# Optimization experiments

Measured on AMD Instinct MI355X. Metric: run time of the kernel, lower is better.

## Reference

```python
import jax, jax.numpy as jnp
import numpy as np

HEADS = 8
EPS = 1e-5


def dwconv(x, w):
    # x: [B, C, L], w: [C, 1, K] depthwise kernel (groups == C), 'same' padding (K odd)
    K = w.shape[-1]
    p = (K - 1) // 2
    return jax.lax.conv_general_dilated(
        x, w, window_strides=(1,), padding=[(p, p)],
        dimension_numbers=('NCH', 'OIH', 'NCH'),
        feature_group_count=x.shape[1])


def dds_conv(x, pw, dw3, dw15, gate):
    # DynamicDepthSeparableConv1d: 1x1 pointwise (no bias) -> two depthwise convs
    # combined with softmax-gated weighted sum.
    o = jnp.einsum('oc,bcl->bol', pw, x)
    g = jax.nn.softmax(gate)
    return g[0] * dwconv(o, dw3) + g[1] * dwconv(o, dw15)


def instance_norm(x, gamma, beta):
    # InstanceNorm1d(affine=True), biased variance over length dim
    m = jnp.mean(x, axis=-1, keepdims=True)
    v = jnp.mean((x - m) ** 2, axis=-1, keepdims=True)
    return (x - m) * jax.lax.rsqrt(v + EPS) * gamma[None, :, None] + beta[None, :, None]


def block(x, p):
    B, C, L = x.shape
    h = HEADS
    Q = dds_conv(x, p['pw_q'], p['dw3_q'], p['dw15_q'], p['gate_q']).reshape(B, h, C, L)
    K = dds_conv(x, p['pw_k'], p['dw3_k'], p['dw15_k'], p['gate_k']).reshape(B, h, C, L)
    V = dds_conv(x, p['pw_v'], p['dw3_v'], p['dw15_v'], p['gate_v']).reshape(B, h, C, L)
    scale = C ** -0.25
    # dot[b,h,k,q] = sum_c K[b,h,c,k] * Q[b,h,c,q]; softmax over key dim (axis=2)
    dot = jnp.einsum('bhck,bhcq->bhkq', K * scale, Q * scale)
    attn = jax.nn.softmax(dot, axis=2)
    o = jnp.einsum('bhck,bhkq->bhcq', V, attn).reshape(B, h * C, L)
    attended = jnp.einsum('oc,bcl->bol', p['uni_W'], o) + p['uni_b'][None, :, None]
    # dropout is identity at inference
    x = instance_norm(attended + x, p['n1_g'], p['n1_b'])
    h1 = jax.nn.relu(jnp.einsum('oc,bcl->bol', p['ffn_W1'], x) + p['ffn_b1'][None, :, None])
    ff = jnp.einsum('oc,bcl->bol', p['ffn_W2'], h1) + p['ffn_b2'][None, :, None]
    x = instance_norm(ff + x, p['n2_g'], p['n2_b'])
    return x


def setup_inputs() -> dict:
    key = jax.random.key(0)
    ks = jax.random.split(key, 32)
    D, C, h, L, B, IN = 6, 32, HEADS, 2048, 8, 6
    CH = C * h
    s = 0.05
    inp = {
        'x': jax.random.normal(ks[0], (B, IN, L), jnp.float32),
        'enc_W': jax.random.normal(ks[1], (C, IN), jnp.float32) * s,
        'enc_b': jnp.zeros((C,), jnp.float32),
        'pw_q': jax.random.normal(ks[2], (D, CH, C), jnp.float32) * s,
        'dw3_q': jax.random.normal(ks[3], (D, CH, 1, 3), jnp.float32) * s,
        'dw15_q': jax.random.normal(ks[4], (D, CH, 1, 15), jnp.float32) * s,
        'gate_q': jnp.ones((D, 2), jnp.float32),
        'pw_k': jax.random.normal(ks[5], (D, CH, C), jnp.float32) * s,
        'dw3_k': jax.random.normal(ks[6], (D, CH, 1, 3), jnp.float32) * s,
        'dw15_k': jax.random.normal(ks[7], (D, CH, 1, 15), jnp.float32) * s,
        'gate_k': jnp.ones((D, 2), jnp.float32),
        'pw_v': jax.random.normal(ks[8], (D, CH, C), jnp.float32) * s,
        'dw3_v': jax.random.normal(ks[9], (D, CH, 1, 3), jnp.float32) * s,
        'dw15_v': jax.random.normal(ks[10], (D, CH, 1, 15), jnp.float32) * s,
        'gate_v': jnp.ones((D, 2), jnp.float32),
        'uni_W': jax.random.normal(ks[11], (D, C, CH), jnp.float32) * s,
        'uni_b': jnp.zeros((D, C), jnp.float32),
        'n1_g': jnp.ones((D, C), jnp.float32),
        'n1_b': jnp.zeros((D, C), jnp.float32),
        'n2_g': jnp.ones((D, C), jnp.float32),
        'n2_b': jnp.zeros((D, C), jnp.float32),
        'ffn_W1': jax.random.normal(ks[12], (D, 4 * C, C), jnp.float32) * s,
        'ffn_b1': jnp.zeros((D, 4 * C), jnp.float32),
        'ffn_W2': jax.random.normal(ks[13], (D, C, 4 * C), jnp.float32) * s,
        'ffn_b2': jnp.zeros((D, C), jnp.float32),
        'cls_W': jax.random.normal(ks[14], (1, C), jnp.float32) * s,
        'cls_b': jnp.zeros((1,), jnp.float32),
    }
    return inp


def reference(x, enc_W, enc_b, pw_q, dw3_q, dw15_q, gate_q, pw_k, dw3_k, dw15_k,
              gate_k, pw_v, dw3_v, dw15_v, gate_v, uni_W, uni_b, n1_g, n1_b,
              n2_g, n2_b, ffn_W1, ffn_b1, ffn_W2, ffn_b2, cls_W, cls_b):
    h = jnp.einsum('oc,bcl->bol', enc_W, x) + enc_b[None, :, None]
    params = dict(pw_q=pw_q, dw3_q=dw3_q, dw15_q=dw15_q, gate_q=gate_q,
                  pw_k=pw_k, dw3_k=dw3_k, dw15_k=dw15_k, gate_k=gate_k,
                  pw_v=pw_v, dw3_v=dw3_v, dw15_v=dw15_v, gate_v=gate_v,
                  uni_W=uni_W, uni_b=uni_b, n1_g=n1_g, n1_b=n1_b,
                  n2_g=n2_g, n2_b=n2_b, ffn_W1=ffn_W1, ffn_b1=ffn_b1,
                  ffn_W2=ffn_W2, ffn_b2=ffn_b2)
    def step(carry, p):
        return block(carry, p), None
    h, _ = jax.lax.scan(step, h, params)
    logits = jnp.einsum('oc,bcl->bol', cls_W, h) + cls_b[None, :, None]  # [B,1,L]
    return jax.nn.sigmoid(logits)[:, 0, :]  # strong (per-timestep) probabilities [B, L]
```

## Files before the change

kernel.cpp:

```cpp
#include <hip/hip_runtime.h>
#include <math.h>

#define LL   2048
#define BB   8
#define CC   32
#define CHH  256
#define HH   8
#define DD   6

typedef _Float16 h8 __attribute__((ext_vector_type(8)));
typedef _Float16 h4 __attribute__((ext_vector_type(4)));
typedef float f4 __attribute__((ext_vector_type(4)));
typedef float f2v __attribute__((ext_vector_type(2)));

__global__ __launch_bounds__(256) void k_enc(const float* __restrict__ x,
    const float* __restrict__ W, const float* __restrict__ bias,
    float* __restrict__ X) {
  int idx = blockIdx.x * 256 + threadIdx.x;
  int l = idx & (LL - 1);
  int c = (idx >> 11) & 31;
  int b = idx >> 16;
  float s = bias[c];
#pragma unroll
  for (int i = 0; i < 6; ++i)
    s = fmaf(W[c * 6 + i], x[((size_t)b * 6 + i) * LL + l], s);
  X[idx] = s;
}

__global__ __launch_bounds__(256) void k_qkv(const float* __restrict__ X,
    const float* __restrict__ pwq, const float* __restrict__ pwk,
    const float* __restrict__ pwv,
    const float* __restrict__ d3q, const float* __restrict__ d15q, const float* __restrict__ gq,
    const float* __restrict__ d3k, const float* __restrict__ d15k, const float* __restrict__ gk,
    const float* __restrict__ d3v, const float* __restrict__ d15v, const float* __restrict__ gv,
    _Float16* __restrict__ Qt, _Float16* __restrict__ Kt, _Float16* __restrict__ Vt) {
  __shared__ __align__(16) char lds[21504];
  int z  = blockIdx.y;
  int bx = blockIdx.x;
  int bh = bx >> 4, lt = bx & 15, l0 = lt * 128;
  int b = bh >> 3, h = bh & 7;
  int t = threadIdx.x;
  const float* pwp  = (z == 0) ? pwq  : (z == 1) ? pwk  : pwv;
  const float* w3p  = (z == 0) ? d3q  : (z == 1) ? d3k  : d3v;
  const float* w15p = (z == 0) ? d15q : (z == 1) ? d15k : d15v;
  const float* gp   = (z == 0) ? gq   : (z == 1) ? gk   : gv;

  char* Xh = lds;
  char* Wh = lds + 9728;
  char* ot = lds + 11776;

  {
    int r = t >> 3, u = t & 7;
    const float* xr = X + ((size_t)b * CC + r) * LL;
    char* xd = Xh + r * 304;
#pragma unroll
    for (int s = u; s < 36; s += 8) {
      int ls = l0 - 8 + s * 4;
      f4 v;
      if (ls >= 0 && ls + 3 < LL) {
        v = *(const f4*)(xr + ls);
      } else {
#pragma unroll
        for (int e = 0; e < 4; ++e) {
          int l = ls + e;
          v[e] = (l >= 0 && l < LL) ? xr[l] : 0.f;
        }
      }
      uint2 pk;
      pk.x = __builtin_bit_cast(unsigned, __builtin_amdgcn_cvt_pkrtz(v[0], v[1]));
      pk.y = __builtin_bit_cast(unsigned, __builtin_amdgcn_cvt_pkrtz(v[2], v[3]));
      *(uint2*)(xd + s * 8) = pk;
    }
  }
  {
    f4 wg = ((const f4*)(pwp + h * 1024))[t];
    uint2 pk;
    pk.x = __builtin_bit_cast(unsigned, __builtin_amdgcn_cvt_pkrtz(wg[0], wg[1]));
    pk.y = __builtin_bit_cast(unsigned, __builtin_amdgcn_cvt_pkrtz(wg[2], wg[3]));
    *(uint2*)(Wh + (t >> 3) * 64 + (t & 7) * 8) = pk;
  }
  __syncthreads();

  {
    int w4 = t >> 6, lane = t & 63;
    int g = lane >> 4, ln = lane & 15;
    h8 af[2];
#pragma unroll
    for (int mt = 0; mt < 2; ++mt)
      af[mt] = *(const h8*)(Wh + (mt * 16 + ln) * 64 + g * 16);
    for (int nt = w4; nt < 9; nt += 4) {
      h8 bf;
#pragma unroll
      for (int j = 0; j < 8; ++j)
        bf[j] = *(const _Float16*)(Xh + (g * 8 + j) * 304 + (nt * 16 + ln) * 2);
#pragma unroll
      for (int mt = 0; mt < 2; ++mt) {
        f4 zr = {0.f, 0.f, 0.f, 0.f};
        f4 d = __builtin_amdgcn_mfma_f32_16x16x32_f16(af[mt], bf, zr, 0, 0, 0);
#pragma unroll
        for (int i = 0; i < 4; ++i)
          *(_Float16*)(ot + (mt * 16 + g * 4 + i) * 304 + (nt * 16 + ln) * 2) =
              (_Float16)d[i];
      }
    }
  }
  __syncthreads();

  int c = t & 31, cg = t >> 5;
  float wv[32];
  {
    const h8* wp = (const h8*)(ot + c * 304 + cg * 32);
#pragma unroll
    for (int q4 = 0; q4 < 4; ++q4) {
      h8 v = wp[q4];
#pragma unroll
      for (int e = 0; e < 8; ++e) wv[q4 * 8 + e] = (float)v[e];
    }
  }
  float r0 = gp[0], r1 = gp[1];
  float mx = fmaxf(r0, r1);
  float e0 = __expf(r0 - mx), e1 = __expf(r1 - mx);
  float gi = 1.f / (e0 + e1);
  float g0 = e0 * gi, g1 = e1 * gi;
  float sc = (z == 0) ? 0.2550765737f : 1.0f;
  int ch = h * 32 + c;
  float w3r[3], w15r[15];
#pragma unroll
  for (int k = 0; k < 3; ++k)  w3r[k]  = w3p[ch * 3 + k];
#pragma unroll
  for (int k = 0; k < 15; ++k) w15r[k] = w15p[ch * 15 + k];

  h8 olo, ohi;
#pragma unroll
  for (int i = 0; i < 16; ++i) {
    float a = 0.f;
#pragma unroll
    for (int k = 0; k < 3; ++k) a = fmaf(w3r[k], wv[i + 7 + k], a);
    float s15 = 0.f;
#pragma unroll
    for (int k = 0; k < 15; ++k) s15 = fmaf(w15r[k], wv[i + 1 + k], s15);
    float val = (g0 * a + g1 * s15) * sc;
    if (i < 8) olo[i] = (_Float16)val; else ohi[i - 8] = (_Float16)val;
  }

  if (z == 2) {
    _Float16* dst = Vt + ((size_t)bh * 32 + c) * LL + l0 + cg * 16;
    *(h8*)dst = olo;
    *(h8*)(dst + 8) = ohi;
  } else {
    char* tb = lds;
    __syncthreads();
#pragma unroll
    for (int i = 0; i < 16; ++i) {
      _Float16 v = (i < 8) ? olo[i] : ohi[i - 8];
      *(_Float16*)(tb + (cg * 16 + i) * 80 + c * 2) = v;
    }
    __syncthreads();
    _Float16* dst = ((z == 0) ? Qt : Kt) + ((size_t)bh * LL + l0) * 32;
    int l = t >> 1, hf = t & 1;
    uint4 a = *(uint4*)(tb + l * 80 + hf * 32);
    uint4 b2 = *(uint4*)(tb + l * 80 + hf * 32 + 16);
    *(uint4*)(dst + (size_t)l * 32 + hf * 16) = a;
    *(uint4*)(dst + (size_t)l * 32 + hf * 16 + 8) = b2;
  }
}

__global__ __launch_bounds__(512, 2) void k_attn(
    const _Float16* __restrict__ Qt, const _Float16* __restrict__ Kt,
    const _Float16* __restrict__ Vt, _Float16* __restrict__ AO) {
  __shared__ __align__(16) char lds[38912];
  const int tid  = threadIdx.x;
  const int lane = tid & 63;
  const int w    = tid >> 6;
  const int seg  = w >> 2;
  const int wq   = w & 3;
  const int g    = lane >> 4;
  const int ln   = lane & 15;
  const int h2c  = (wq >> 1) * 2;
  const int lin  = blockIdx.x + (blockIdx.y << 4);
  const int swz  = ((lin & 7) << 7) | (lin >> 3);
  const int qb   = swz & 15;
  const int bh   = swz >> 4;
  const _Float16* Qg = Qt + ((size_t)bh * LL + qb * 128) * 32;
  const _Float16* Kg = Kt + ((size_t)bh * LL + seg * 1024) * 32;
  const _Float16* Vg = Vt + (size_t)bh * 32 * LL + seg * 1024;

  h8 qf[2];
#pragma unroll
  for (int nt = 0; nt < 2; ++nt)
    qf[nt] = *(const h8*)(Qg + (size_t)(wq * 32 + nt * 16 + ln) * 32 + g * 8);

  h8 ones;
#pragma unroll
  for (int j = 0; j < 8; ++j) ones[j] = (_Float16)1.0f;

  char* kb = lds + seg * 5120;
  char* vb = lds + 20480 + seg * 4608;

  uint4 stg0, stg1;
  if ((wq & 1) == 0) {
    const uint4* gk = (const uint4*)Kg;
    stg0 = gk[h2c * 64 + lane];
    stg1 = gk[(h2c + 1) * 64 + lane];
    *(uint4*)(kb + (h2c * 16 + (lane >> 2)) * 80 + (lane & 3) * 16) = stg0;
    *(uint4*)(kb + ((h2c + 1) * 16 + (lane >> 2)) * 80 + (lane & 3) * 16) = stg1;
  } else {
    int c0 = h2c * 8 + (lane >> 3);
    stg0 = *(const uint4*)(Vg + (size_t)c0 * LL + (lane & 7) * 8);
    stg1 = *(const uint4*)(Vg + (size_t)(c0 + 8) * LL + (lane & 7) * 8);
    *(uint4*)(vb + c0 * 144 + (lane & 7) * 16) = stg0;
    *(uint4*)(vb + (c0 + 8) * 144 + (lane & 7) * 16) = stg1;
  }
  __syncthreads();

  f4 o[2][2];
#pragma unroll
  for (int ct = 0; ct < 2; ++ct)
#pragma unroll
    for (int nt = 0; nt < 2; ++nt) o[ct][nt] = (f4){0.f, 0.f, 0.f, 0.f};
  f4 sacc[2];
#pragma unroll
  for (int nt = 0; nt < 2; ++nt) sacc[nt] = (f4){0.f, 0.f, 0.f, 0.f};

  for (int it = 0; it < 16; ++it) {
    int pp = it & 1;
    char* kbc = kb + pp * 10240;
    char* vbc = vb + pp * 9216;
    if (it < 15) {
      int k0n = (it + 1) * 64;
      if ((wq & 1) == 0) {
        const uint4* gk = (const uint4*)(Kg + (size_t)k0n * 32);
        stg0 = gk[h2c * 64 + lane];
        stg1 = gk[(h2c + 1) * 64 + lane];
      } else {
        int c0 = h2c * 8 + (lane >> 3);
        stg0 = *(const uint4*)(Vg + (size_t)c0 * LL + k0n + (lane & 7) * 8);
        stg1 = *(const uint4*)(Vg + (size_t)(c0 + 8) * LL + k0n + (lane & 7) * 8);
      }
    }
#pragma unroll
    for (int chunk = 0; chunk < 2; ++chunk) {
      unsigned pa[2][2], pb[2][2];
#pragma unroll
      for (int mt2 = 0; mt2 < 2; ++mt2) {
        h8 kf = *(const h8*)(kbc + ((chunk * 2 + mt2) * 16 + ln) * 80 + g * 16);
#pragma unroll
        for (int nt = 0; nt < 2; ++nt) {
          f4 z = {0.f, 0.f, 0.f, 0.f};
          f4 s = __builtin_amdgcn_mfma_f32_16x16x32_f16(kf, qf[nt], z, 0, 0, 0);
          float p0 = __builtin_amdgcn_exp2f(s[0]);
          float p1 = __builtin_amdgcn_exp2f(s[1]);
          float p2 = __builtin_amdgcn_exp2f(s[2]);
          float p3 = __builtin_amdgcn_exp2f(s[3]);
          unsigned lo = __builtin_bit_cast(unsigned,
              __builtin_amdgcn_cvt_pkrtz(p0, p1));
          unsigned hi = __builtin_bit_cast(unsigned,
              __builtin_amdgcn_cvt_pkrtz(p2, p3));
          if (mt2 == 0) { pa[nt][0] = lo; pa[nt][1] = hi; }
          else          { pb[nt][0] = lo; pb[nt][1] = hi; }
        }
      }
      h8 vf[2];
#pragma unroll
      for (int ct = 0; ct < 2; ++ct)
        vf[ct] = *(const h8*)(vbc + (ct * 16 + ln) * 144 + chunk * 64 + g * 16);
#pragma unroll
      for (int nt = 0; nt < 2; ++nt) {
        unsigned w0 = pa[nt][0], w1 = pa[nt][1];
        unsigned w2 = pb[nt][0], w3 = pb[nt][1];
        asm("v_permlane32_swap_b32 %0, %1" : "+v"(w0), "+v"(w2));
        asm("v_permlane16_swap_b32 %0, %1" : "+v"(w0), "+v"(w2));
        asm("v_permlane32_swap_b32 %0, %1" : "+v"(w1), "+v"(w3));
        asm("v_permlane16_swap_b32 %0, %1" : "+v"(w1), "+v"(w3));
        uint4 pw4; pw4.x = w0; pw4.y = w1; pw4.z = w2; pw4.w = w3;
        h8 pf = __builtin_bit_cast(h8, pw4);
        sacc[nt] = __builtin_amdgcn_mfma_f32_16x16x32_f16(ones, pf, sacc[nt], 0, 0, 0);
        o[0][nt] = __builtin_amdgcn_mfma_f32_16x16x32_f16(vf[0], pf, o[0][nt], 0, 0, 0);
        o[1][nt] = __builtin_amdgcn_mfma_f32_16x16x32_f16(vf[1], pf, o[1][nt], 0, 0, 0);
      }
    }
    if (it < 15) {
      char* kbn = kb + (pp ^ 1) * 10240;
      char* vbn = vb + (pp ^ 1) * 9216;
      if ((wq & 1) == 0) {
        *(uint4*)(kbn + (h2c * 16 + (lane >> 2)) * 80 + (lane & 3) * 16) = stg0;
        *(uint4*)(kbn + ((h2c + 1) * 16 + (lane >> 2)) * 80 + (lane & 3) * 16) = stg1;
      } else {
        int c0 = h2c * 8 + (lane >> 3);
        *(uint4*)(vbn + c0 * 144 + (lane & 7) * 16) = stg0;
        *(uint4*)(vbn + (c0 + 8) * 144 + (lane & 7) * 16) = stg1;
      }
    }
    __syncthreads();
  }

  if (seg == 1) {
    char* eo = lds + wq * 9216 + lane * 144;
#pragma unroll
    for (int nt = 0; nt < 2; ++nt)
#pragma unroll
      for (int ct = 0; ct < 2; ++ct)
        *(f4*)(eo + (nt * 2 + ct) * 16) = o[ct][nt];
    f4 sv;
    sv[0] = sacc[0][0]; sv[1] = sacc[1][0];
    sv[2] = 0.f; sv[3] = 0.f;
    *(f4*)(eo + 64) = sv;
  }
  __syncthreads();
  if (seg == 0) {
    const char* po = lds + wq * 9216 + lane * 144;
    f4 s1v = *(const f4*)(po + 64);
    _Float16* out = AO + (size_t)bh * (32 * LL);
#pragma unroll
    for (int nt = 0; nt < 2; ++nt) {
      float inv = 1.f / (sacc[nt][0] + s1v[nt]);
      int qg = qb * 128 + wq * 32 + nt * 16 + ln;
#pragma unroll
      for (int ct = 0; ct < 2; ++ct) {
        f4 o1 = *(const f4*)(po + (nt * 2 + ct) * 16);
#pragma unroll
        for (int r = 0; r < 4; ++r)
          out[(size_t)(ct * 16 + g * 4 + r) * LL + qg] =
              (_Float16)((o[ct][nt][r] + o1[r]) * inv);
      }
    }
  }
}

__global__ __launch_bounds__(256) void k_uni_res(const _Float16* __restrict__ AO,
    const float* __restrict__ W, const float* __restrict__ bias,
    const float* __restrict__ Xin, float* __restrict__ Y) {
  __shared__ __align__(16) char lds[35840];
  char* Wh = lds;
  char* Bh = lds + 17920;
  int t  = threadIdx.x;
  int bx = blockIdx.x;
  int lt = bx & 63, b = bx >> 6;
  int l0 = lt * 32;

#pragma unroll
  for (int i = 0; i < 8; ++i) {
    int idx = t + i * 256;
    f4 wv4 = ((const f4*)W)[idx];
    uint2 pk;
    pk.x = __builtin_bit_cast(unsigned, __builtin_amdgcn_cvt_pkrtz(wv4[0], wv4[1]));
    pk.y = __builtin_bit_cast(unsigned, __builtin_amdgcn_cvt_pkrtz(wv4[2], wv4[3]));
    int c = idx >> 6, ccp = idx & 63;
    *(uint2*)(Wh + c * 560 + ccp * 8) = pk;
  }
#pragma unroll
  for (int it = 0; it < 4; ++it) {
    int cc = it * 64 + (t >> 2), chunk = t & 3;
    h8 av = *(const h8*)(AO + ((size_t)b * CHH + cc) * LL + l0 + chunk * 8);
#pragma unroll
    for (int e = 0; e < 8; ++e)
      *(_Float16*)(Bh + (chunk * 8 + e) * 560 + cc * 2) = av[e];
  }
  __syncthreads();

  int wv = t >> 6, lane = t & 63;
  int g = lane >> 4, ln = lane & 15;
  int mt = wv >> 1, nt2 = wv & 1;
  f4 acc = {0.f, 0.f, 0.f, 0.f};
#pragma unroll
  for (int ks = 0; ks < 8; ++ks) {
    h8 af = *(const h8*)(Wh + (mt * 16 + ln) * 560 + (ks * 32 + g * 8) * 2);
    h8 bf = *(const h8*)(Bh + (nt2 * 16 + ln) * 560 + (ks * 32 + g * 8) * 2);
    acc = __builtin_amdgcn_mfma_f32_16x16x32_f16(af, bf, acc, 0, 0, 0);
  }
#pragma unroll
  for (int i = 0; i < 4; ++i) {
    int c = mt * 16 + g * 4 + i;
    size_t o = ((size_t)b * CC + c) * LL + l0 + nt2 * 16 + ln;
    Y[o] = acc[i] + bias[c] + Xin[o];
  }
}

__global__ __launch_bounds__(512) void k_inorm(const float* __restrict__ Y,
    float* __restrict__ X, const float* __restrict__ g,
    const float* __restrict__ bt) {
  __shared__ float red[16];
  int row = blockIdx.x;
  int c = row & 31;
  const float* y = Y + (size_t)row * LL;
  float v[4];
  float s = 0.f, ss = 0.f;
#pragma unroll
  for (int i = 0; i < 4; ++i) {
    v[i] = y[threadIdx.x + 512 * i];
    s += v[i];
    ss = fmaf(v[i], v[i], ss);
  }
#pragma unroll
  for (int off = 32; off; off >>= 1) {
    s  += __shfl_down(s, off);
    ss += __shfl_down(ss, off);
  }
  int wid = threadIdx.x >> 6;
  if ((threadIdx.x & 63) == 0) { red[wid * 2] = s; red[wid * 2 + 1] = ss; }
  __syncthreads();
  if (threadIdx.x == 0) {
    float rs0 = 0.f, rs1 = 0.f;
#pragma unroll
    for (int i = 0; i < 8; ++i) { rs0 += red[i * 2]; rs1 += red[i * 2 + 1]; }
    red[0] = rs0; red[1] = rs1;
  }
  __syncthreads();
  float mean = red[0] * (1.f / LL);
  float var  = red[1] * (1.f / LL) - mean * mean;
  float rs = rsqrtf(var + 1e-5f) * g[c];
  float bb = bt[c];
#pragma unroll
  for (int i = 0; i < 4; ++i)
    X[(size_t)row * LL + threadIdx.x + 512 * i] = (v[i] - mean) * rs + bb;
}

__global__ __launch_bounds__(256) void k_ffn(const float* __restrict__ X,
    const float* __restrict__ W1, const float* __restrict__ b1,
    const float* __restrict__ W2, const float* __restrict__ b2,
    float* __restrict__ Y) {
  __shared__ __align__(16) char lds[30720];
  char* Xh  = lds;
  char* W1h = lds + 2560;
  char* W2h = lds + 12800;
  char* Hh  = lds + 21504;
  float* b1h = (float*)(lds + 30208);
  int t  = threadIdx.x;
  int bx = blockIdx.x;
  int lt = bx & 63, b = bx >> 6;
  int l0 = lt * 32;

  {
    int c = t >> 3, le0 = (t & 7) * 4;
    f4 v = *(const f4*)(X + ((size_t)b * CC + c) * LL + l0 + le0);
#pragma unroll
    for (int e = 0; e < 4; ++e)
      *(_Float16*)(Xh + (le0 + e) * 80 + c * 2) = (_Float16)v[e];
  }
#pragma unroll
  for (int i = 0; i < 4; ++i) {
    int idx = t + i * 256;
    f4 wv4 = ((const f4*)W1)[idx];
    uint2 pk;
    pk.x = __builtin_bit_cast(unsigned, __builtin_amdgcn_cvt_pkrtz(wv4[0], wv4[1]));
    pk.y = __builtin_bit_cast(unsigned, __builtin_amdgcn_cvt_pkrtz(wv4[2], wv4[3]));
    int o = idx >> 3, cp = idx & 7;
    *(uint2*)(W1h + o * 80 + cp * 8) = pk;
  }
#pragma unroll
  for (int i = 0; i < 4; ++i) {
    int idx = t + i * 256;
    f4 wv4 = ((const f4*)W2)[idx];
    uint2 pk;
    pk.x = __builtin_bit_cast(unsigned, __builtin_amdgcn_cvt_pkrtz(wv4[0], wv4[1]));
    pk.y = __builtin_bit_cast(unsigned, __builtin_amdgcn_cvt_pkrtz(wv4[2], wv4[3]));
    int c = idx >> 5, op = idx & 31;
    *(uint2*)(W2h + c * 272 + op * 8) = pk;
  }
  if (t < 128) b1h[t] = b1[t];
  __syncthreads();

  int w4 = t >> 6, lane = t & 63;
  int g = lane >> 4, ln = lane & 15;

#pragma unroll
  for (int j = 0; j < 4; ++j) {
    int ti = w4 * 4 + j;
    int ot = ti >> 1, lt2 = ti & 1;
    h8 af = *(const h8*)(W1h + (ot * 16 + ln) * 80 + g * 16);
    h8 bf = *(const h8*)(Xh + (lt2 * 16 + ln) * 80 + g * 16);
    f4 zr = {0.f, 0.f, 0.f, 0.f};
    f4 d = __builtin_amdgcn_mfma_f32_16x16x32_f16(af, bf, zr, 0, 0, 0);
#pragma unroll
    for (int i = 0; i < 4; ++i) {
      int o = ot * 16 + g * 4 + i;
      float hv = fmaxf(d[i] + b1h[o], 0.f);
      *(_Float16*)(Hh + (lt2 * 16 + ln) * 272 + o * 2) = (_Float16)hv;
    }
  }
  __syncthreads();

  int ct2 = w4 >> 1, lt2b = w4 & 1;
  f4 acc = {0.f, 0.f, 0.f, 0.f};
#pragma unroll
  for (int ks = 0; ks < 4; ++ks) {
    h8 af = *(const h8*)(W2h + (ct2 * 16 + ln) * 272 + (ks * 32 + g * 8) * 2);
    h8 bf = *(const h8*)(Hh + (lt2b * 16 + ln) * 272 + (ks * 32 + g * 8) * 2);
    acc = __builtin_amdgcn_mfma_f32_16x16x32_f16(af, bf, acc, 0, 0, 0);
  }
#pragma unroll
  for (int i = 0; i < 4; ++i) {
    int c = ct2 * 16 + g * 4 + i;
    size_t o = ((size_t)b * CC + c) * LL + l0 + lt2b * 16 + ln;
    Y[o] = acc[i] + b2[c] + X[o];
  }
}

__global__ __launch_bounds__(256) void k_cls(const float* __restrict__ X,
    const float* __restrict__ W, const float* __restrict__ bias,
    float* __restrict__ out) {
  int idx = blockIdx.x * 256 + threadIdx.x;
  int l = idx & (LL - 1);
  int b = idx >> 11;
  float s = bias[0];
#pragma unroll
  for (int c = 0; c < CC; ++c)
    s = fmaf(W[c], X[((size_t)b * CC + c) * LL + l], s);
  out[idx] = 1.f / (1.f + __expf(-s));
}

extern "C" void kernel_launch(void* const* d_in, const int* in_sizes, int n_in,
                              void* d_out, int out_size, void* d_ws,
                              size_t ws_size, hipStream_t stream) {
  const float* x      = (const float*)d_in[0];
  const float* enc_W  = (const float*)d_in[1];
  const float* enc_b  = (const float*)d_in[2];
  const float* pw_q   = (const float*)d_in[3];
  const float* dw3_q  = (const float*)d_in[4];
  const float* dw15_q = (const float*)d_in[5];
  const float* gate_q = (const float*)d_in[6];
  const float* pw_k   = (const float*)d_in[7];
  const float* dw3_k  = (const float*)d_in[8];
  const float* dw15_k = (const float*)d_in[9];
  const float* gate_k = (const float*)d_in[10];
  const float* pw_v   = (const float*)d_in[11];
  const float* dw3_v  = (const float*)d_in[12];
  const float* dw15_v = (const float*)d_in[13];
  const float* gate_v = (const float*)d_in[14];
  const float* uni_W  = (const float*)d_in[15];
  const float* uni_b  = (const float*)d_in[16];
  const float* n1_g   = (const float*)d_in[17];
  const float* n1_b   = (const float*)d_in[18];
  const float* n2_g   = (const float*)d_in[19];
  const float* n2_b   = (const float*)d_in[20];
  const float* ffn_W1 = (const float*)d_in[21];
  const float* ffn_b1 = (const float*)d_in[22];
  const float* ffn_W2 = (const float*)d_in[23];
  const float* ffn_b2 = (const float*)d_in[24];
  const float* cls_W  = (const float*)d_in[25];
  const float* cls_b  = (const float*)d_in[26];

  float* ws = (float*)d_ws;
  float* X   = ws;
  float* Y   = ws + 524288;
  _Float16* AO = (_Float16*)(ws + 1048576);
  _Float16* Qt = (_Float16*)(ws + 9437184);
  _Float16* Kt = (_Float16*)(ws + 11534336);
  _Float16* Vt = (_Float16*)(ws + 13631488);

  k_enc<<<2048, 256, 0, stream>>>(x, enc_W, enc_b, X);

  for (int d = 0; d < DD; ++d) {
    k_qkv<<<dim3(1024, 3), 256, 0, stream>>>(X,
        pw_q + d * CHH * CC, pw_k + d * CHH * CC, pw_v + d * CHH * CC,
        dw3_q + d * CHH * 3, dw15_q + d * CHH * 15, gate_q + d * 2,
        dw3_k + d * CHH * 3, dw15_k + d * CHH * 15, gate_k + d * 2,
        dw3_v + d * CHH * 3, dw15_v + d * CHH * 15, gate_v + d * 2,
        Qt, Kt, Vt);
    k_attn<<<dim3(16, 64), 512, 0, stream>>>(Qt, Kt, Vt, AO);
    k_uni_res<<<512, 256, 0, stream>>>(AO, uni_W + d * CC * CHH,
                                       uni_b + d * CC, X, Y);
    k_inorm<<<256, 512, 0, stream>>>(Y, X, n1_g + d * CC, n1_b + d * CC);
    k_ffn<<<512, 256, 0, stream>>>(X, ffn_W1 + d * 128 * CC, ffn_b1 + d * 128,
                                   ffn_W2 + d * CC * 128, ffn_b2 + d * CC, Y);
    k_inorm<<<256, 512, 0, stream>>>(Y, X, n2_g + d * CC, n2_b + d * CC);
  }

  k_cls<<<64, 256, 0, stream>>>(X, cls_W, cls_b, (float*)d_out);
}
```

Measured before the change: 610.5 us.

## Fuse instance norm into producer/consumer kernels via atomic per-row statistics

Removes the two standalone instance-norm kernels per layer. The residual-producing kernels now accumulate per-(batch,channel) sum and sum-of-squares with shuffle reductions and atomics. The consuming kernels (qkv, ffn, cls) apply the normalization as a scale/shift when they load their input. This cuts 12 launches and the extra read/write passes over the activations, at the cost of atomic contention, a memset, and the less stable E[x^2]-mean^2 variance computed from atomically summed partials.

```diff
diff --git a/kernel.cpp b/kernel.cpp
--- a/kernel.cpp
+++ b/kernel.cpp
@@ -12,6 +12,15 @@
 typedef _Float16 h4 __attribute__((ext_vector_type(4)));
 typedef float f4 __attribute__((ext_vector_type(4)));
 typedef float f2v __attribute__((ext_vector_type(2)));
+
+__device__ __forceinline__ void norm_params(const float* st, const float* g,
+    const float* bt, int bc, int c, float& scr, float& shr) {
+  float s0 = st[bc * 2], s1 = st[bc * 2 + 1];
+  float mean = s0 * (1.f / LL);
+  float var  = s1 * (1.f / LL) - mean * mean;
+  float q = rsqrtf(var + 1e-5f) * g[c];
+  scr = q; shr = bt[c] - mean * q;
+}
 
 __global__ __launch_bounds__(256) void k_enc(const float* __restrict__ x,
     const float* __restrict__ W, const float* __restrict__ bias,
@@ -27,7 +36,9 @@
   X[idx] = s;
 }
 
-__global__ __launch_bounds__(256) void k_qkv(const float* __restrict__ X,
+__global__ __launch_bounds__(256) void k_qkv(const float* __restrict__ Xin,
+    const float* __restrict__ stin, const float* __restrict__ ng,
+    const float* __restrict__ nb, int hasn,
     const float* __restrict__ pwq, const float* __restrict__ pwk,
     const float* __restrict__ pwv,
     const float* __restrict__ d3q, const float* __restrict__ d15q, const float* __restrict__ gq,
@@ -51,7 +62,9 @@
 
   {
     int r = t >> 3, u = t & 7;
-    const float* xr = X + ((size_t)b * CC + r) * LL;
+    const float* xr = Xin + ((size_t)b * CC + r) * LL;
+    float scr = 1.f, shr = 0.f;
+    if (hasn) norm_params(stin, ng, nb, b * 32 + r, r, scr, shr);
     char* xd = Xh + r * 304;
 #pragma unroll
     for (int s = u; s < 36; s += 8) {
@@ -59,11 +72,13 @@
       f4 v;
       if (ls >= 0 && ls + 3 < LL) {
         v = *(const f4*)(xr + ls);
+#pragma unroll
+        for (int e = 0; e < 4; ++e) v[e] = fmaf(v[e], scr, shr);
       } else {
 #pragma unroll
         for (int e = 0; e < 4; ++e) {
           int l = ls + e;
-          v[e] = (l >= 0 && l < LL) ? xr[l] : 0.f;
+          v[e] = (l >= 0 && l < LL) ? fmaf(xr[l], scr, shr) : 0.f;
         }
       }
       uint2 pk;
@@ -329,10 +344,14 @@
 
 __global__ __launch_bounds__(256) void k_uni_res(const _Float16* __restrict__ AO,
     const float* __restrict__ W, const float* __restrict__ bias,
-    const float* __restrict__ Xin, float* __restrict__ Y) {
-  __shared__ __align__(16) char lds[35840];
+    const float* __restrict__ Ain, const float* __restrict__ stin,
+    const float* __restrict__ png, const float* __restrict__ pnb, int hasn,
+    float* __restrict__ Y, float* __restrict__ stout) {
+  __shared__ __align__(16) char lds[36096];
   char* Wh = lds;
   char* Bh = lds + 17920;
+  float* nsc = (float*)(lds + 35840);
+  float* nsh = nsc + 32;
   int t  = threadIdx.x;
   int bx = blockIdx.x;
   int lt = bx & 63, b = bx >> 6;
@@ -356,6 +375,11 @@
     for (int e = 0; e < 8; ++e)
       *(_Float16*)(Bh + (chunk * 8 + e) * 560 + cc * 2) = av[e];
   }
+  if (t < 32) {
+    float scr = 1.f, shr = 0.f;
+    if (hasn) norm_params(stin, png, pnb, b * 32 + t, t, scr, shr);
+    nsc[t] = scr; nsh[t] = shr;
+  }
   __syncthreads();
 
   int wv = t >> 6, lane = t & 63;
@@ -372,59 +396,36 @@
   for (int i = 0; i < 4; ++i) {
     int c = mt * 16 + g * 4 + i;
     size_t o = ((size_t)b * CC + c) * LL + l0 + nt2 * 16 + ln;
-    Y[o] = acc[i] + bias[c] + Xin[o];
-  }
-}
-
-__global__ __launch_bounds__(512) void k_inorm(const float* __restrict__ Y,
-    float* __restrict__ X, const float* __restrict__ g,
-    const float* __restrict__ bt) {
-  __shared__ float red[16];
-  int row = blockIdx.x;
-  int c = row & 31;
-  const float* y = Y + (size_t)row * LL;
-  float v[4];
-  float s = 0.f, ss = 0.f;
-#pragma unroll
-  for (int i = 0; i < 4; ++i) {
-    v[i] = y[threadIdx.x + 512 * i];
-    s += v[i];
-    ss = fmaf(v[i], v[i], ss);
-  }
-#pragma unroll
-  for (int off = 32; off; off >>= 1) {
-    s  += __shfl_down(s, off);
-    ss += __shfl_down(ss, off);
-  }
-  int wid = threadIdx.x >> 6;
-  if ((threadIdx.x & 63) == 0) { red[wid * 2] = s; red[wid * 2 + 1] = ss; }
-  __syncthreads();
-  if (threadIdx.x == 0) {
-    float rs0 = 0.f, rs1 = 0.f;
-#pragma unroll
-    for (int i = 0; i < 8; ++i) { rs0 += red[i * 2]; rs1 += red[i * 2 + 1]; }
-    red[0] = rs0; red[1] = rs1;
-  }
-  __syncthreads();
-  float mean = red[0] * (1.f / LL);
-  float var  = red[1] * (1.f / LL) - mean * mean;
-  float rs = rsqrtf(var + 1e-5f) * g[c];
-  float bb = bt[c];
-#pragma unroll
-  for (int i = 0; i < 4; ++i)
-    X[(size_t)row * LL + threadIdx.x + 512 * i] = (v[i] - mean) * rs + bb;
-}
-
-__global__ __launch_bounds__(256) void k_ffn(const float* __restrict__ X,
+    float res = fmaf(Ain[o], nsc[c], nsh[c]);
+    float val = acc[i] + bias[c] + res;
+    Y[o] = val;
+    float a = val, v2 = val * val;
+#pragma unroll
+    for (int off = 8; off; off >>= 1) {
+      a  += __shfl_down(a, off, 16);
+      v2 += __shfl_down(v2, off, 16);
+    }
+    if (ln == 0) {
+      atomicAdd(&stout[(b * 32 + c) * 2], a);
+      atomicAdd(&stout[(b * 32 + c) * 2 + 1], v2);
+    }
+  }
+}
+
+__global__ __launch_bounds__(256) void k_ffn(const float* __restrict__ Y1,
+    const float* __restrict__ st1, const float* __restrict__ n1g,
+    const float* __restrict__ n1b,
     const float* __restrict__ W1, const float* __restrict__ b1,
     const float* __restrict__ W2, const float* __restrict__ b2,
-    float* __restrict__ Y) {
-  __shared__ __align__(16) char lds[30720];
+    float* __restrict__ Y2, float* __restrict__ stout) {
+  __shared__ __align__(16) char lds[31232];
   char* Xh  = lds;
   char* W1h = lds + 2560;
   char* W2h = lds + 12800;
   char* Hh  = lds + 21504;
   float* b1h = (float*)(lds + 30208);
+  float* nsc = (float*)(lds + 30720);
+  float* nsh = nsc + 32;
   int t  = threadIdx.x;
   int bx = blockIdx.x;
   int lt = bx & 63, b = bx >> 6;
@@ -432,10 +433,13 @@
 
   {
     int c = t >> 3, le0 = (t & 7) * 4;
-    f4 v = *(const f4*)(X + ((size_t)b * CC + c) * LL + l0 + le0);
+    float scr, shr;
+    norm_params(st1, n1g, n1b, b * 32 + c, c, scr, shr);
+    if ((t & 7) == 0) { nsc[c] = scr; nsh[c] = shr; }
+    f4 v = *(const f4*)(Y1 + ((size_t)b * CC + c) * LL + l0 + le0);
 #pragma unroll
     for (int e = 0; e < 4; ++e)
-      *(_Float16*)(Xh + (le0 + e) * 80 + c * 2) = (_Float16)v[e];
+      *(_Float16*)(Xh + (le0 + e) * 80 + c * 2) = (_Float16)fmaf(v[e], scr, shr);
   }
 #pragma unroll
   for (int i = 0; i < 4; ++i) {
@@ -492,20 +496,43 @@
   for (int i = 0; i < 4; ++i) {
     int c = ct2 * 16 + g * 4 + i;
     size_t o = ((size_t)b * CC + c) * LL + l0 + lt2b * 16 + ln;
-    Y[o] = acc[i] + b2[c] + X[o];
-  }
-}
-
-__global__ __launch_bounds__(256) void k_cls(const float* __restrict__ X,
+    float xn = fmaf(Y1[o], nsc[c], nsh[c]);
+    float val = acc[i] + b2[c] + xn;
+    Y2[o] = val;
+    float a = val, v2 = val * val;
+#pragma unroll
+    for (int off = 8; off; off >>= 1) {
+      a  += __shfl_down(a, off, 16);
+      v2 += __shfl_down(v2, off, 16);
+    }
+    if (ln == 0) {
+      atomicAdd(&stout[(b * 32 + c) * 2], a);
+      atomicAdd(&stout[(b * 32 + c) * 2 + 1], v2);
+    }
+  }
+}
+
+__global__ __launch_bounds__(256) void k_cls(const float* __restrict__ Y2,
+    const float* __restrict__ st2, const float* __restrict__ n2g,
+    const float* __restrict__ n2b,
     const float* __restrict__ W, const float* __restrict__ bias,
     float* __restrict__ out) {
+  __shared__ float nsc[32], nsh[32];
   int idx = blockIdx.x * 256 + threadIdx.x;
   int l = idx & (LL - 1);
   int b = idx >> 11;
+  if (threadIdx.x < 32) {
+    float scr, shr;
+    norm_params(st2, n2g, n2b, b * 32 + threadIdx.x, threadIdx.x, scr, shr);
+    nsc[threadIdx.x] = scr; nsh[threadIdx.x] = shr;
+  }
+  __syncthreads();
   float s = bias[0];
 #pragma unroll
-  for (int c = 0; c < CC; ++c)
-    s = fmaf(W[c], X[((size_t)b * CC + c) * LL + l], s);
+  for (int c = 0; c < CC; ++c) {
+    float xn = fmaf(Y2[((size_t)b * CC + c) * LL + l], nsc[c], nsh[c]);
+    s = fmaf(W[c], xn, s);
+  }
   out[idx] = 1.f / (1.f + __expf(-s));
 }
 
@@ -541,17 +568,27 @@
   const float* cls_b  = (const float*)d_in[26];
 
   float* ws = (float*)d_ws;
-  float* X   = ws;
-  float* Y   = ws + 524288;
+  float* X0  = ws;
+  float* Y1  = ws + 524288;
   _Float16* AO = (_Float16*)(ws + 1048576);
+  float* Y2  = ws + 3145728;
   _Float16* Qt = (_Float16*)(ws + 9437184);
   _Float16* Kt = (_Float16*)(ws + 11534336);
   _Float16* Vt = (_Float16*)(ws + 13631488);
-
-  k_enc<<<2048, 256, 0, stream>>>(x, enc_W, enc_b, X);
+  float* st1 = ws + 15728640;
+  float* st2 = st1 + 3072;
+
+  hipMemsetAsync(st1, 0, 6144 * sizeof(float), stream);
+
+  k_enc<<<2048, 256, 0, stream>>>(x, enc_W, enc_b, X0);
 
   for (int d = 0; d < DD; ++d) {
-    k_qkv<<<dim3(1024, 3), 256, 0, stream>>>(X,
+    const float* Ain = (d == 0) ? X0 : Y2;
+    const float* stA = (d == 0) ? nullptr : st2 + (d - 1) * 512;
+    const float* g2  = (d == 0) ? n2_g : n2_g + (d - 1) * CC;
+    const float* b2p = (d == 0) ? n2_b : n2_b + (d - 1) * CC;
+    int hasn = (d != 0);
+    k_qkv<<<dim3(1024, 3), 256, 0, stream>>>(Ain, stA, g2, b2p, hasn,
         pw_q + d * CHH * CC, pw_k + d * CHH * CC, pw_v + d * CHH * CC,
         dw3_q + d * CHH * 3, dw15_q + d * CHH * 15, gate_q + d * 2,
         dw3_k + d * CHH * 3, dw15_k + d * CHH * 15, gate_k + d * 2,
@@ -559,12 +596,12 @@
         Qt, Kt, Vt);
     k_attn<<<dim3(16, 64), 512, 0, stream>>>(Qt, Kt, Vt, AO);
     k_uni_res<<<512, 256, 0, stream>>>(AO, uni_W + d * CC * CHH,
-                                       uni_b + d * CC, X, Y);
-    k_inorm<<<256, 512, 0, stream>>>(Y, X, n1_g + d * CC, n1_b + d * CC);
-    k_ffn<<<512, 256, 0, stream>>>(X, ffn_W1 + d * 128 * CC, ffn_b1 + d * 128,
-                                   ffn_W2 + d * CC * 128, ffn_b2 + d * CC, Y);
-    k_inorm<<<256, 512, 0, stream>>>(Y, X, n2_g + d * CC, n2_b + d * CC);
-  }
-
-  k_cls<<<64, 256, 0, stream>>>(X, cls_W, cls_b, (float*)d_out);
-}
+        uni_b + d * CC, Ain, stA, g2, b2p, hasn, Y1, st1 + d * 512);
+    k_ffn<<<512, 256, 0, stream>>>(Y1, st1 + d * 512, n1_g + d * CC,
+        n1_b + d * CC, ffn_W1 + d * 128 * CC, ffn_b1 + d * 128,
+        ffn_W2 + d * CC * 128, ffn_b2 + d * CC, Y2, st2 + d * 512);
+  }
+
+  k_cls<<<64, 256, 0, stream>>>(Y2, st2 + 5 * 512, n2_g + 5 * CC,
+                                n2_b + 5 * CC, cls_W, cls_b, (float*)d_out);
+}
```

Measured after the change: 873.0 us. +43.0%, slower.
